# Optimization experiments

Hardware: AMD Instinct MI355X
Metric: run time of the kernel (lower is better)

Reference implementation:

```python
import jax, jax.numpy as jnp
import numpy as np

B = 16            # batch of graphs
N = 512           # n_node
D = 32            # embedding_dim
MAXN = 16         # max_neighbors
E = MAXN * (N - 1)   # 8176 edges per graph
SLEFT = N * D
FSS = 601         # full_support_size
NA = N - 1        # num_actions (so one-hot rows == B*n_node)
IN0 = D + 1       # sa feature dim
NTOT = B * N


def _gat(x, snd, rcv, W, a_src, a_dst, b):
    # single-head GATConv, add_self_loops=False
    h = x @ W                                            # [BN, C]
    e = (h * a_src).sum(-1)[snd] + (h * a_dst).sum(-1)[rcv]
    e = jnp.where(e > 0, e, 0.2 * e)                     # LeakyReLU(0.2)
    m = jax.ops.segment_max(e, rcv, num_segments=NTOT)   # segment softmax
    m = jnp.where(jnp.isfinite(m), m, 0.0)
    ee = jnp.exp(e - m[rcv])
    den = jax.ops.segment_sum(ee, rcv, num_segments=NTOT)
    alpha = ee / (den[rcv] + 1e-16)
    return jax.ops.segment_sum(alpha[:, None] * h[snd], rcv, num_segments=NTOT) + b


def _ln(x, s, o):
    # hk.LayerNorm(axis=-2): normalize over node axis, scale/offset over features
    x3 = x.reshape(B, N, -1)
    mu = x3.mean(axis=1, keepdims=True)
    var = ((x3 - mu) ** 2).mean(axis=1, keepdims=True)
    return ((x3 - mu) * jax.lax.rsqrt(var + 1e-5) * s + o).reshape(B * N, -1)


def _gat_params(key, din, dout):
    k1, k2, k3 = jax.random.split(key, 3)
    sc = 1.0 / np.sqrt(din)
    return (jax.random.normal(k1, (din, dout), jnp.float32) * sc,
            jax.random.normal(k2, (dout,), jnp.float32) * sc,
            jax.random.normal(k3, (dout,), jnp.float32) * sc,
            jnp.zeros((dout,), jnp.float32))


def setup_inputs():
    key = jax.random.key(0)
    ks = jax.random.split(key, 4)
    nodes = jax.random.normal(ks[0], (B, SLEFT), jnp.float32)
    snd = jax.random.randint(ks[1], (B, E), 0, N).astype(jnp.float32)
    rcv = jax.random.randint(ks[2], (B, E), 0, N).astype(jnp.float32)
    ns = jnp.concatenate([nodes, snd, rcv], axis=1)      # [B, SLEFT + 2E]
    a = jax.random.randint(ks[3], (B,), 0, NA + 1)
    inp = {"ns": ns, "a": a}
    dims = [(IN0, 4 * D), (4 * D, 2 * D), (2 * D, 2 * D), (2 * D, D)]
    rdims = [(IN0, FSS), (FSS, FSS), (FSS, FSS), (FSS, FSS)]
    for i, (di, do) in enumerate(dims, 1):
        W, asrc, adst, b = _gat_params(jax.random.fold_in(key, 100 + i), di, do)
        inp.update({f"W{i}": W, f"a{i}s": asrc, f"a{i}d": adst, f"b{i}": b})
        if i < 4:
            inp.update({f"s{i}": jnp.ones((do,), jnp.float32), f"o{i}": jnp.zeros((do,), jnp.float32)})
    for i, (di, do) in enumerate(rdims, 1):
        W, asrc, adst, b = _gat_params(jax.random.fold_in(key, 200 + i), di, do)
        inp.update({f"rW{i}": W, f"ra{i}s": asrc, f"ra{i}d": adst, f"rb{i}": b})
        if i < 4:
            inp.update({f"rs{i}": jnp.ones((FSS,), jnp.float32), f"ro{i}": jnp.zeros((FSS,), jnp.float32)})
    return inp


def reference(ns, a,
              W1, a1s, a1d, b1, s1, o1,
              W2, a2s, a2d, b2, s2, o2,
              W3, a3s, a3d, b3, s3, o3,
              W4, a4s, a4d, b4,
              rW1, ra1s, ra1d, rb1, rs1, ro1,
              rW2, ra2s, ra2d, rb2, rs2, ro2,
              rW3, ra3s, ra3d, rb3, rs3, ro3,
              rW4, ra4s, ra4d, rb4):
    # gbatch: offset per-graph indices into one big graph
    off = (jnp.arange(B, dtype=jnp.int32) * N)[:, None]
    snd = (ns[:, SLEFT:SLEFT + E].astype(jnp.int32) + off).reshape(-1)
    rcv = (ns[:, SLEFT + E:SLEFT + 2 * E].astype(jnp.int32) + off).reshape(-1)
    nodes = ns[:, :SLEFT].reshape(B * N, D)
    sa = jnp.concatenate([nodes, jax.nn.one_hot(a, NA + 1).reshape(-1, 1)], axis=1)
    # reward head
    r = jax.nn.relu(_ln(_gat(sa, snd, rcv, rW1, ra1s, ra1d, rb1), rs1, ro1))
    r = jax.nn.relu(_ln(_gat(r, snd, rcv, rW2, ra2s, ra2d, rb2), rs2, ro2))
    r = jax.nn.relu(_ln(_gat(r, snd, rcv, rW3, ra3s, ra3d, rb3), rs3, ro3))
    r = _gat(r, snd, rcv, rW4, ra4s, ra4d, rb4).reshape(B, N, FSS).sum(axis=1)
    # next-state head
    f = jax.nn.relu(_ln(_gat(sa, snd, rcv, W1, a1s, a1d, b1), s1, o1))
    f = jax.nn.relu(_ln(_gat(f, snd, rcv, W2, a2s, a2d, b2), s2, o2))
    f = jax.nn.relu(_ln(_gat(f, snd, rcv, W3, a3s, a3d, b3), s3, o3))
    f = _gat(f, snd, rcv, W4, a4s, a4d, b4).reshape(B, N * D)
    ns_new = jnp.concatenate([f, ns[:, SLEFT:]], axis=1)
    return (r, ns_new)
```

## Files before the change

### kernel.cpp

```cpp
#include <hip/hip_runtime.h>
#include <math.h>

#define B_ 16
#define N_ 512
#define D_ 32
#define E_ 8176
#define SLEFT_ 16384
#define FSS_ 601
#define BN_ (B_*N_)
#define BE_ (B_*E_)
#define NSROW_ (SLEFT_ + 2*E_)
#define OUT_R_ (B_*FSS_)
#define HLD_ 768
#define CAP_ 128
#define KXB_ 736

typedef __attribute__((ext_vector_type(8))) short short8;
typedef __attribute__((ext_vector_type(4))) float f32x4;

typedef __attribute__((address_space(3))) uint lds_uint;
typedef __attribute__((address_space(1))) const uint g_uint;

__device__ __forceinline__ void gl_lds16(const ushort* gp, ushort* lp) {
  __builtin_amdgcn_global_load_lds((g_uint*)gp, (lds_uint*)lp, 16, 0, 0);
}

__device__ __forceinline__ ushort f2b(float f) {
  uint u = __builtin_bit_cast(uint, f);
  u += 0x7FFFu + ((u >> 16) & 1u);
  return (ushort)(u >> 16);
}
__device__ __forceinline__ float b2f(ushort h) {
  return __builtin_bit_cast(float, ((uint)h) << 16);
}


struct SetupP {
  const float* ns; const int* a;
  int* cnt; int* bins; ushort* sa; float* outp;
  const float* Wr[4]; const float* Wn[4]; ushort* T[4];
};

__global__ __launch_bounds__(256) void k_setup(SetupP p) {
  __shared__ float tile[32][33];
  int blk = blockIdx.x;
  if (blk < 511) {
    int idx = blk*256 + threadIdx.x;
    if (idx >= BE_) return;
    int b = idx / E_;
    int j = idx - b*E_;
    const float* row = p.ns + (size_t)b*NSROW_;
    int s = (int)row[SLEFT_ + j];
    int r = (int)row[SLEFT_ + E_ + j];
    int dst = b*N_ + r;
    int pos = atomicAdd(&p.cnt[dst], 1);
    if (pos < CAP_) p.bins[(size_t)dst*CAP_ + pos] = b*N_ + s;
    return;
  }
  if (blk < 767) {
    int it = (blk-511)*256 + threadIdx.x;
    int v = it >> 3, c0 = (it & 7) * 8;
    int b = v >> 9, n = v & 511;
    short8 ov;
    if (c0 < 32) {
      const float* src = p.ns + (size_t)b*NSROW_ + n*32 + c0;
      #pragma unroll
      for (int j=0;j<8;j++) ov[j] = (short)f2b(src[j]);
    } else {
      #pragma unroll
      for (int j=0;j<8;j++) ov[j] = 0;
      if (c0 == 32) ov[0] = (short)f2b((p.a[b]==n) ? 1.f : 0.f);
    }
    *(short8*)&p.sa[(size_t)v*64 + c0] = ov;
    return;
  }
  if (blk < 1023) {
    int it = (blk-767)*256 + threadIdx.x;
    int b = it >> 12;
    int r = it & 4095;
    if (r < (NSROW_ - SLEFT_)/4) {
      const float4* src = (const float4*)(p.ns + (size_t)b*NSROW_ + SLEFT_) + r;
      float4* dst = (float4*)(p.outp + (size_t)OUT_R_ + (size_t)b*NSROW_ + SLEFT_) + r;
      *dst = *src;
    }
    return;
  }
  int t = blk - 1023;
  int s, base, KP, DINR, DINN, DOUTN, KOFF;
  if (t < 48)        { s=0; base=0;    KP=64;  DINR=33;  DINN=33;  DOUTN=128; KOFF=0;   }
  else if (t < 600)  { s=1; base=48;   KP=736; DINR=601; DINN=128; DOUTN=64;  KOFF=608; }
  else if (t < 1104) { s=2; base=600;  KP=672; DINR=601; DINN=64;  DOUTN=64;  KOFF=608; }
  else               { s=3; base=1104; KP=672; DINR=601; DINN=64;  DOUTN=32;  KOFF=608; }
  int ti = t - base;
  int kt = ti / 24, nt = ti - kt*24;
  int k0 = kt*32, n0 = nt*32;
  if (k0 >= KP) return;
  int tid = threadIdx.x;
  int cc = tid & 31, rr = tid >> 5;
  #pragma unroll
  for (int it=0; it<4; it++) {
    int k = k0 + it*8 + rr;
    int n = n0 + cc;
    float v = 0.f;
    if (n < 640) { if (n < 601 && k < DINR) v = p.Wr[s][(size_t)k*601 + n]; }
    else { int nn = n-640, kk = k-KOFF;
           if (nn < DOUTN && kk >= 0 && kk < DINN) v = p.Wn[s][(size_t)kk*DOUTN + nn]; }
    tile[it*8+rr][cc] = v;
  }
  __syncthreads();
  #pragma unroll
  for (int it=0; it<4; it++) {
    int n = n0 + it*8 + rr;
    int k = k0 + cc;
    p.T[s][(size_t)n*KP + k] = f2b(tile[cc][it*8+rr]);
  }
}


__global__ __launch_bounds__(256) void k_gemm(const ushort* __restrict__ A,
                                              const ushort* __restrict__ Bt,
                                              ushort* __restrict__ C,
                                              float* __restrict__ esed,
                                              const float* __restrict__ asr,
                                              const float* __restrict__ adr,
                                              const float* __restrict__ asn,
                                              const float* __restrict__ adn,
                                              int Astr, int Kpad, int dn,
                                              int kRewEnd, int kNextBeg) {
  __shared__ ushort Asm[64*32];
  __shared__ ushort Bsm[128*32];
  int tid = threadIdx.x;
  int bid = blockIdx.x;
  int x = bid & 7, q = bid >> 3;
  int rbl = q & 15, cb = q >> 4;
  int grp = x + ((rbl >> 3) << 3);
  int rowBase = (grp*8 + (rbl & 7)) * 64;
  int colBase = cb * 128;
  int kBeg = (cb == 5) ? kNextBeg : 0;
  int kEnd = (cb == 5) ? Kpad : kRewEnd;
  int wave = tid >> 6, lane = tid & 63;
  int wr = (wave >> 1) * 32, wc = (wave & 1) * 64;
  int lm = lane & 15, lk = (lane >> 4) * 8;

  f32x4 acc[2][4];
  #pragma unroll
  for (int i=0;i<2;i++)
    #pragma unroll
    for (int j=0;j<4;j++) acc[i][j] = (f32x4){0.f,0.f,0.f,0.f};

  int t0 = tid, t1 = tid + 256;
  int ar = t0 >> 2, ac8 = (t0 & 3) * 8;
  const ushort* Bg0 = Bt + (size_t)(colBase + (t0>>2))*Kpad + (t0&3)*8;
  const ushort* Bg1 = Bt + (size_t)(colBase + (t1>>2))*Kpad + (t1&3)*8;
  ushort* Bl0 = &Bsm[t0*8];
  ushort* Bl1 = &Bsm[t1*8];
  ushort* Al0 = &Asm[t0*8];

  const ushort* Ag = A + (size_t)(rowBase + ar)*Astr + ac8;

  for (int k0 = kBeg; k0 < kEnd; k0 += 32) {
    gl_lds16(Bg0 + k0, Bl0);
    gl_lds16(Bg1 + k0, Bl1);
    gl_lds16(Ag + k0, Al0);
    __syncthreads();
    short8 af[2], bfr[4];
    #pragma unroll
    for (int i=0;i<2;i++) af[i]  = *(short8*)&Asm[(wr + i*16 + lm)*32 + lk];
    #pragma unroll
    for (int j=0;j<4;j++) bfr[j] = *(short8*)&Bsm[(wc + j*16 + lm)*32 + lk];
    #pragma unroll
    for (int i=0;i<2;i++)
      #pragma unroll
      for (int j=0;j<4;j++)
        acc[i][j] = __builtin_amdgcn_mfma_f32_16x16x32_bf16(af[i], bfr[j], acc[i][j], 0,0,0);
    __syncthreads();
  }

  float asv[4], adv[4];
  #pragma unroll
  for (int j=0;j<4;j++) {
    int col = colBase + wc + j*16 + lm;
    float s = 0.f, d = 0.f;
    if (col < 601)      { s = asr[col];     d = adr[col]; }
    else if (col >= 640 && col - 640 < dn) { s = asn[col-640]; d = adn[col-640]; }
    asv[j] = s; adv[j] = d;
  }
  int cr = lane >> 4;
  int ct2 = cb*2 + (wc >> 6);
  float* esp = (ct2 < 10) ? esed : esed + 2*BN_;
  #pragma unroll
  for (int i=0;i<2;i++) {
    #pragma unroll
    for (int j=0;j<4;j++) {
      int col = colBase + wc + j*16 + lm;
      #pragma unroll
      for (int g=0; g<4; g++) {
        int row = rowBase + wr + i*16 + cr*4 + g;
        C[(size_t)row*HLD_ + col] = f2b(acc[i][j][g]);
      }
    }
    #pragma unroll
    for (int g=0; g<4; g++) {
      float se = 0.f, sd = 0.f;
      #pragma unroll
      for (int j=0;j<4;j++) { se += acc[i][j][g]*asv[j]; sd += acc[i][j][g]*adv[j]; }
      #pragma unroll
      for (int o=1;o<16;o<<=1) { se += __shfl_xor(se,o,64); sd += __shfl_xor(sd,o,64); }
      if (lm == 0) {
        int row = rowBase + wr + i*16 + cr*4 + g;
        atomicAdd(&esp[row], se);
        atomicAdd(&esp[BN_ + row], sd);
      }
    }
  }
}


__global__ __launch_bounds__(256) void k_agg(const ushort* __restrict__ h,
                                             const float* __restrict__ esed,
                                             const int* __restrict__ cnt,
                                             const int* __restrict__ bins,
                                             const float* __restrict__ bias_r,
                                             const float* __restrict__ bias_n,
                                             ushort* __restrict__ g,
                                             float* __restrict__ outp,
                                             int dn, int doRsum) {
  __shared__ float RW[4][608];
  const float* es_r = esed;
  const float* ed_r = esed + BN_;
  const float* es_n = esed + 2*BN_;
  const float* ed_n = esed + 3*BN_;
  int wid = threadIdx.x>>6, lane = threadIdx.x&63;
  int bid = blockIdx.x;
  int xcd = bid & 7, slot = bid >> 3;
  int graph = xcd + ((slot >> 7) << 3);
  int nloc = (slot & 127)*4 + wid;
  int v = graph*512 + nloc;
  int s0 = v * CAP_;
  int deg = cnt[v]; if (deg > CAP_) deg = CAP_;
  float edr = ed_r[v], edn = ed_n[v];

  int nch = (640 + dn + 7) >> 3;
  int ch0 = lane, ch1 = lane + 64;
  bool a1 = ch1 < nch;
  bool c1r = ch1 < 80;
  float acc0[8], acc1[8];
  #pragma unroll
  for (int q=0;q<8;q++){ acc0[q]=0.f; acc1[q]=0.f; }

  if (deg <= 64) {
    bool has = lane < deg;
    int u = 0; float er = -__builtin_inff(), en = -__builtin_inff();
    if (has) {
      u = bins[s0 + lane];
      er = es_r[u] + edr; er = er > 0.f ? er : 0.2f*er;
      en = es_n[u] + edn; en = en > 0.f ? en : 0.2f*en;
    }
    float mr = er, mn = en;
    #pragma unroll
    for (int o=32;o;o>>=1) { mr = fmaxf(mr, __shfl_xor(mr,o,64)); mn = fmaxf(mn, __shfl_xor(mn,o,64)); }
    float pr = has ? __expf(er - mr) : 0.f;
    float pn = has ? __expf(en - mn) : 0.f;
    float dr = pr, dnm = pn;
    #pragma unroll
    for (int o=32;o;o>>=1) { dr += __shfl_xor(dr,o,64); dnm += __shfl_xor(dnm,o,64); }
    pr *= 1.f/(dr + 1e-16f);
    pn *= 1.f/(dnm + 1e-16f);

    for (int t0 = 0; t0 < deg; t0 += 4) {
      int nt = deg - t0; if (nt > 4) nt = 4;
      short8 va[4], vb[4];
      float w0[4], w1[4];
      #pragma unroll
      for (int q=0;q<4;q++) {
        if (q < nt) {
          int uu = __shfl(u, t0+q, 64);
          w0[q] = __shfl(pr, t0+q, 64);
          w1[q] = __shfl(pn, t0+q, 64);
          const ushort* hp = h + (size_t)uu*HLD_;
          va[q] = *(const short8*)&hp[ch0*8];
          vb[q] = a1 ? *(const short8*)&hp[ch1*8] : short8{};
        } else {
          w0[q] = 0.f; w1[q] = 0.f; va[q] = short8{}; vb[q] = short8{};
        }
      }
      #pragma unroll
      for (int q=0;q<4;q++) {
        #pragma unroll
        for (int r=0;r<8;r++) acc0[r] += w0[q] * b2f((ushort)va[q][r]);
        if (a1) {
          float wv = c1r ? w0[q] : w1[q];
          #pragma unroll
          for (int r=0;r<8;r++) acc1[r] += wv * b2f((ushort)vb[q][r]);
        }
      }
    }
  } else {
    int e0 = s0 + deg;
    float mr = -__builtin_inff(), mn = -__builtin_inff();
    for (int j = s0 + lane; j < e0; j += 64) {
      int u = bins[j];
      float er = es_r[u] + edr; er = er>0.f?er:0.2f*er;
      float en = es_n[u] + edn; en = en>0.f?en:0.2f*en;
      mr = fmaxf(mr, er); mn = fmaxf(mn, en);
    }
    #pragma unroll
    for (int o=32;o;o>>=1) { mr=fmaxf(mr,__shfl_xor(mr,o,64)); mn=fmaxf(mn,__shfl_xor(mn,o,64)); }
    float dr=0.f, dnm=0.f;
    for (int j = s0 + lane; j < e0; j += 64) {
      int u = bins[j];
      float er = es_r[u] + edr; er = er>0.f?er:0.2f*er;
      float en = es_n[u] + edn; en = en>0.f?en:0.2f*en;
      dr += __expf(er-mr); dnm += __expf(en-mn);
    }
    #pragma unroll
    for (int o=32;o;o>>=1) { dr+=__shfl_xor(dr,o,64); dnm+=__shfl_xor(dnm,o,64); }
    float ir = 1.f/(dr+1e-16f), in_ = 1.f/(dnm+1e-16f);
    for (int j = s0; j < e0; ++j) {
      int uu = bins[j];
      float er = es_r[uu] + edr; er = er>0.f?er:0.2f*er;
      float en = es_n[uu] + edn; en = en>0.f?en:0.2f*en;
      float wr2 = __expf(er-mr)*ir, wn2 = __expf(en-mn)*in_;
      const ushort* hp = h + (size_t)uu*HLD_;
      short8 hv = *(const short8*)&hp[ch0*8];
      #pragma unroll
      for (int q=0;q<8;q++) acc0[q] += wr2 * b2f((ushort)hv[q]);
      if (a1) {
        short8 hv2 = *(const short8*)&hp[ch1*8];
        float wv = c1r ? wr2 : wn2;
        #pragma unroll
        for (int q=0;q<8;q++) acc1[q] += wv * b2f((ushort)hv2[q]);
      }
    }
  }

  ushort* gv = g + (size_t)v*HLD_;
  {
    int cb = ch0*8;
    short8 ov;
    #pragma unroll
    for (int q=0;q<8;q++) ov[q] = (short)f2b(acc0[q] + bias_r[cb+q]);
    if (!doRsum) {
      *(short8*)&gv[cb] = ov;
    } else {
      #pragma unroll
      for (int q=0;q<8;q++) RW[wid][cb+q] = b2f((ushort)ov[q]);
    }
  }
  if (a1) {
    int cb = ch1*8;
    short8 ov;
    #pragma unroll
    for (int q=0;q<8;q++) {
      int c = cb+q;
      float val;
      if (c < 601)                         val = acc1[q] + bias_r[c];
      else if (c >= 640 && (c-640) < dn)   val = acc1[q] + bias_n[c-640];
      else                                 val = 0.f;
      ov[q] = (short)f2b(val);
    }
    if (!doRsum) {
      *(short8*)&gv[cb] = ov;
    } else {
      if (cb < 608) {
        #pragma unroll
        for (int q=0;q<8;q++) {
          int c = cb+q;
          RW[wid][c] = (c < 601) ? b2f((ushort)ov[q]) : 0.f;
        }
      }
      #pragma unroll
      for (int q=0;q<8;q++) {
        int c = cb+q;
        if (c >= 640 && (c-640) < dn) {
          outp[(size_t)OUT_R_ + (size_t)graph*NSROW_ + nloc*D_ + (c-640)] =
              b2f((ushort)ov[q]);
        }
      }
    }
  }
  if (doRsum) {
    if (!a1 && ch1*8 < 608) {
      #pragma unroll
      for (int q=0;q<8;q++) RW[wid][ch1*8+q] = 0.f;
    }
    __syncthreads();
    for (int c = threadIdx.x; c < 601; c += 256) {
      float s = RW[0][c] + RW[1][c] + RW[2][c] + RW[3][c];
      atomicAdd(&outp[(size_t)graph*FSS_ + c], s);
    }
  }
}


__global__ __launch_bounds__(256) void k_lnfin(const ushort* __restrict__ g,
                                               const float* __restrict__ scr,
                                               const float* __restrict__ ofr,
                                               const float* __restrict__ scn,
                                               const float* __restrict__ ofn,
                                               ushort* __restrict__ xbuf,
                                               int dn) {
  int bid = blockIdx.x;
  int x = bid & 7, sl = bid >> 3;
  int b = x + ((sl >= 12) ? 8 : 0);
  int cbk = (sl >= 12) ? (sl - 12) : sl;
  int t = threadIdx.x;
  int c8l = t & 7;
  int rg  = t >> 3;
  int xb8 = cbk*64 + c8l*8;
  bool okc = xb8 < KXB_;
  int gcol8 = (xb8 < 608) ? xb8 : xb8 + 32;
  float s8[8], q8[8];
  #pragma unroll
  for (int j=0;j<8;j++){ s8[j]=0.f; q8[j]=0.f; }
  if (okc) {
    const ushort* gp = g + (size_t)(b*N_ + rg*16)*HLD_ + gcol8;
    #pragma unroll
    for (int i=0;i<16;i++) {
      short8 v = *(const short8*)&gp[(size_t)i*HLD_];
      #pragma unroll
      for (int j=0;j<8;j++) {
        float xv = b2f((ushort)v[j]);
        s8[j] += xv; q8[j] += xv*xv;
      }
    }
  }
  __shared__ float S[32][64], Q[32][64];
  __shared__ float MU[64], AD[64];
  #pragma unroll
  for (int j=0;j<8;j++){ S[rg][c8l*8+j]=s8[j]; Q[rg][c8l*8+j]=q8[j]; }
  __syncthreads();
  if (t < 64) {
    int xb = cbk*64 + t;
    float mul = 0.f, add = 0.f;
    if (xb < KXB_) {
      float ts=0.f, tq=0.f;
      #pragma unroll
      for (int r=0;r<32;r++){ ts += S[r][t]; tq += Q[r][t]; }
      bool valid; float scale, offs;
      if (xb < 608) { valid = xb < 601;
                      scale = valid ? scr[xb] : 0.f; offs = valid ? ofr[xb] : 0.f; }
      else { int cn = xb - 608; valid = cn < dn;
             scale = valid ? scn[cn] : 0.f; offs = valid ? ofn[cn] : 0.f; }
      if (valid) {
        float mu = ts*(1.f/N_);
        float var = tq*(1.f/N_) - mu*mu;
        float rs = rsqrtf(var+1e-5f);
        mul = rs*scale;
        add = offs - mu*rs*scale;
      }
    }
    MU[t] = mul; AD[t] = add;
  }
  __syncthreads();
  if (okc) {
    float mu8[8], ad8[8];
    #pragma unroll
    for (int j=0;j<8;j++){ mu8[j]=MU[c8l*8+j]; ad8[j]=AD[c8l*8+j]; }
    const ushort* gp = g + (size_t)(b*N_ + rg*16)*HLD_ + gcol8;
    ushort* xp = xbuf + (size_t)(b*N_ + rg*16)*KXB_ + xb8;
    #pragma unroll
    for (int i=0;i<16;i++) {
      short8 v = *(const short8*)&gp[(size_t)i*HLD_];
      short8 ov;
      #pragma unroll
      for (int j=0;j<8;j++) {
        float y = b2f((ushort)v[j]) * mu8[j] + ad8[j];
        y = y > 0.f ? y : 0.f;
        ov[j] = (short)f2b(y);
      }
      *(short8*)&xp[(size_t)i*KXB_] = ov;
    }
  }
}


extern "C" void kernel_launch(void* const* d_in, const int* in_sizes, int n_in,
                              void* d_out, int out_size, void* d_ws, size_t ws_size,
                              hipStream_t stream) {
  const float* ns = (const float*)d_in[0];
  const int*   a  = (const int*)d_in[1];

  const float *W[4], *As[4], *Ad[4], *Bb[4], *Sc[3], *Of[3];
  const float *rW[4], *rAs[4], *rAd[4], *rBb[4], *rSc[3], *rOf[3];
  int p = 2;
  for (int i=0;i<4;i++){
    W[i]=(const float*)d_in[p++]; As[i]=(const float*)d_in[p++];
    Ad[i]=(const float*)d_in[p++]; Bb[i]=(const float*)d_in[p++];
    if (i<3){ Sc[i]=(const float*)d_in[p++]; Of[i]=(const float*)d_in[p++]; }
  }
  for (int i=0;i<4;i++){
    rW[i]=(const float*)d_in[p++]; rAs[i]=(const float*)d_in[p++];
    rAd[i]=(const float*)d_in[p++]; rBb[i]=(const float*)d_in[p++];
    if (i<3){ rSc[i]=(const float*)d_in[p++]; rOf[i]=(const float*)d_in[p++]; }
  }

  char* w = (char*)d_ws;
  auto carve = [&](size_t bytes)->void* {
    void* r = (void*)w;
    w += (bytes + 255) & ~(size_t)255;
    return r;
  };
  ushort* hbuf = (ushort*)carve((size_t)BN_*HLD_*2);
  ushort* gbuf = (ushort*)carve((size_t)BN_*HLD_*2);
  ushort* xbuf = (ushort*)carve((size_t)BN_*KXB_*2);
  ushort* sabf = (ushort*)carve((size_t)BN_*64*2);
  int* cnt     = (int*)carve((size_t)(BN_ + 16*BN_)*4);
  float* esedL = (float*)(cnt + BN_);
  int* bins    = (int*)carve((size_t)BN_*CAP_*4);
  ushort* Wt[4];
  Wt[0] = (ushort*)carve((size_t)768*64*2);
  Wt[1] = (ushort*)carve((size_t)768*736*2);
  Wt[2] = (ushort*)carve((size_t)768*672*2);
  Wt[3] = (ushort*)carve((size_t)768*672*2);

  float* out = (float*)d_out;

  hipMemsetAsync(cnt, 0, (size_t)(BN_ + 16*BN_)*4, stream);
  hipMemsetAsync(out, 0, (size_t)OUT_R_*4, stream);

  SetupP sp;
  sp.ns = ns; sp.a = a; sp.cnt = cnt; sp.bins = bins; sp.sa = sabf; sp.outp = out;
  for (int i=0;i<4;i++){ sp.Wr[i]=rW[i]; sp.Wn[i]=W[i]; sp.T[i]=Wt[i]; }
  k_setup<<<2631, 256, 0, stream>>>(sp);

  int Kp[4]   = { 64, 736, 672, 672 };
  int dns[4]  = { 128, 64, 64, 32 };
  int kRe[4]  = { 64, 608, 608, 608 };
  int kNb[4]  = { 0, 608, 608, 608 };

  for (int L=0; L<4; ++L) {
    float* esed = esedL + (size_t)L*4*BN_;
    const ushort* Ain = (L==0) ? sabf : xbuf;
    int Astr        = (L==0) ? 64 : KXB_;
    k_gemm<<<768, 256, 0, stream>>>(Ain, Wt[L], hbuf, esed,
                                    rAs[L], rAd[L], As[L], Ad[L],
                                    Astr, Kp[L], dns[L], kRe[L], kNb[L]);
    k_agg<<<BN_/4, 256, 0, stream>>>(hbuf, esed, cnt, bins,
                                     rBb[L], Bb[L], gbuf, out,
                                     dns[L], (L==3)?1:0);
    if (L < 3) {
      k_lnfin<<<192, 256, 0, stream>>>(gbuf, rSc[L], rOf[L], Sc[L], Of[L],
                                       xbuf, dns[L]);
    }
  }
}
```

Before: 334.2 us.

## Load GEMM operands directly into registers with software prefetch, drop LDS staging

The bf16 MFMA GEMM no longer stages A and B tiles through shared memory with global_load_lds and two barriers per k-step. Each lane now reads its fragments straight from global memory into registers, and the next k-step's fragments are prefetched while the current MFMAs run. This removes LDS traffic and block-wide synchronisation. The cost is duplicated global reads across waves that share rows or columns, which now rely on cache instead of LDS reuse, plus higher register pressure.

```diff
diff --git a/kernel.cpp b/kernel.cpp
--- a/kernel.cpp
+++ b/kernel.cpp
@@ -20,10 +20,6 @@
 
 typedef __attribute__((address_space(3))) uint lds_uint;
 typedef __attribute__((address_space(1))) const uint g_uint;
-
-__device__ __forceinline__ void gl_lds16(const ushort* gp, ushort* lp) {
-  __builtin_amdgcn_global_load_lds((g_uint*)gp, (lds_uint*)lp, 16, 0, 0);
-}
 
 __device__ __forceinline__ ushort f2b(float f) {
   uint u = __builtin_bit_cast(uint, f);
@@ -127,8 +123,6 @@
                                               const float* __restrict__ adn,
                                               int Astr, int Kpad, int dn,
                                               int kRewEnd, int kNextBeg) {
-  __shared__ ushort Asm[64*32];
-  __shared__ ushort Bsm[128*32];
   int tid = threadIdx.x;
   int bid = blockIdx.x;
   int x = bid & 7, q = bid >> 3;
@@ -148,32 +142,37 @@
     #pragma unroll
     for (int j=0;j<4;j++) acc[i][j] = (f32x4){0.f,0.f,0.f,0.f};
 
-  int t0 = tid, t1 = tid + 256;
-  int ar = t0 >> 2, ac8 = (t0 & 3) * 8;
-  const ushort* Bg0 = Bt + (size_t)(colBase + (t0>>2))*Kpad + (t0&3)*8;
-  const ushort* Bg1 = Bt + (size_t)(colBase + (t1>>2))*Kpad + (t1&3)*8;
-  ushort* Bl0 = &Bsm[t0*8];
-  ushort* Bl1 = &Bsm[t1*8];
-  ushort* Al0 = &Asm[t0*8];
-
-  const ushort* Ag = A + (size_t)(rowBase + ar)*Astr + ac8;
+  const ushort* Ap0 = A  + (size_t)(rowBase + wr      + lm)*Astr + lk;
+  const ushort* Ap1 = A  + (size_t)(rowBase + wr + 16 + lm)*Astr + lk;
+  const ushort* Bp0 = Bt + (size_t)(colBase + wc      + lm)*Kpad + lk;
+  const ushort* Bp1 = Bt + (size_t)(colBase + wc + 16 + lm)*Kpad + lk;
+  const ushort* Bp2 = Bt + (size_t)(colBase + wc + 32 + lm)*Kpad + lk;
+  const ushort* Bp3 = Bt + (size_t)(colBase + wc + 48 + lm)*Kpad + lk;
+
+  short8 a0 = *(const short8*)(Ap0 + kBeg);
+  short8 a1 = *(const short8*)(Ap1 + kBeg);
+  short8 b0 = *(const short8*)(Bp0 + kBeg);
+  short8 b1 = *(const short8*)(Bp1 + kBeg);
+  short8 b2 = *(const short8*)(Bp2 + kBeg);
+  short8 b3 = *(const short8*)(Bp3 + kBeg);
 
   for (int k0 = kBeg; k0 < kEnd; k0 += 32) {
-    gl_lds16(Bg0 + k0, Bl0);
-    gl_lds16(Bg1 + k0, Bl1);
-    gl_lds16(Ag + k0, Al0);
-    __syncthreads();
-    short8 af[2], bfr[4];
-    #pragma unroll
-    for (int i=0;i<2;i++) af[i]  = *(short8*)&Asm[(wr + i*16 + lm)*32 + lk];
-    #pragma unroll
-    for (int j=0;j<4;j++) bfr[j] = *(short8*)&Bsm[(wc + j*16 + lm)*32 + lk];
-    #pragma unroll
-    for (int i=0;i<2;i++)
-      #pragma unroll
-      for (int j=0;j<4;j++)
-        acc[i][j] = __builtin_amdgcn_mfma_f32_16x16x32_bf16(af[i], bfr[j], acc[i][j], 0,0,0);
-    __syncthreads();
+    int kn = (k0 + 32 < kEnd) ? (k0 + 32) : k0;
+    short8 na0 = *(const short8*)(Ap0 + kn);
+    short8 na1 = *(const short8*)(Ap1 + kn);
+    short8 nb0 = *(const short8*)(Bp0 + kn);
+    short8 nb1 = *(const short8*)(Bp1 + kn);
+    short8 nb2 = *(const short8*)(Bp2 + kn);
+    short8 nb3 = *(const short8*)(Bp3 + kn);
+    acc[0][0] = __builtin_amdgcn_mfma_f32_16x16x32_bf16(a0, b0, acc[0][0], 0,0,0);
+    acc[0][1] = __builtin_amdgcn_mfma_f32_16x16x32_bf16(a0, b1, acc[0][1], 0,0,0);
+    acc[0][2] = __builtin_amdgcn_mfma_f32_16x16x32_bf16(a0, b2, acc[0][2], 0,0,0);
+    acc[0][3] = __builtin_amdgcn_mfma_f32_16x16x32_bf16(a0, b3, acc[0][3], 0,0,0);
+    acc[1][0] = __builtin_amdgcn_mfma_f32_16x16x32_bf16(a1, b0, acc[1][0], 0,0,0);
+    acc[1][1] = __builtin_amdgcn_mfma_f32_16x16x32_bf16(a1, b1, acc[1][1], 0,0,0);
+    acc[1][2] = __builtin_amdgcn_mfma_f32_16x16x32_bf16(a1, b2, acc[1][2], 0,0,0);
+    acc[1][3] = __builtin_amdgcn_mfma_f32_16x16x32_bf16(a1, b3, acc[1][3], 0,0,0);
+    a0 = na0; a1 = na1; b0 = nb0; b1 = nb1; b2 = nb2; b3 = nb3;
   }
 
   float asv[4], adv[4];
```

Measured after the change: 375.5 us. +12.3%, slower.
